# Kernel optimization log

Hardware: AMD Instinct MI355X
Metric: run time of the kernel (lower is better)

The kernel has to match this reference:

```python
import jax, jax.numpy as jnp
import numpy as np

DIM = 4096
N_HEADS = 32
N_KV_HEADS = 8
HEAD_DIM = 128
N_REP = N_HEADS // N_KV_HEADS  # 4
Q_DIM = N_HEADS * HEAD_DIM     # 4096
K_DIM = N_KV_HEADS * HEAD_DIM  # 1024
B, T = 2, 2048
ROPE_THETA = 10000.0


def setup_inputs() -> dict:
    key = jax.random.key(0)
    k1, k2, k3, k4 = jax.random.split(key, 4)
    x = jax.random.normal(k1, (B, T, DIM), dtype=jnp.float32)
    wqkv = jax.random.normal(k2, (Q_DIM + 2 * K_DIM, DIM), dtype=jnp.float32) * 0.02
    wo = jax.random.normal(k3, (DIM, DIM), dtype=jnp.float32) * 0.02
    # RoPE tables: [max_T, head_dim//2]
    inv_freq = 1.0 / (ROPE_THETA ** (jnp.arange(0, HEAD_DIM, 2, dtype=jnp.float32) / HEAD_DIM))
    angles = jnp.arange(T, dtype=jnp.float32)[:, None] * inv_freq[None, :]  # [T, D/2]
    cos = jnp.cos(angles)
    sin = jnp.sin(angles)
    freqs_cis = jax.random.normal(k4, (T, HEAD_DIM // 2), dtype=jnp.float32)  # unused by forward
    return {"x": x, "freqs_cis": freqs_cis, "wqkv": wqkv, "wo": wo, "cos": cos, "sin": sin}


def _apply_rope(q, k, cos, sin):
    # q: [B,T,Hq,D], k: [B,T,Hkv,D]; interleaved even/odd pairs
    Tlen = q.shape[1]
    c = cos[:Tlen][None, :, None, :]  # [1,T,1,D/2]
    s = sin[:Tlen][None, :, None, :]

    def rot(t):
        tr, ti = t[..., 0::2], t[..., 1::2]
        or_ = tr * c - ti * s
        oi = tr * s + ti * c
        return jnp.stack([or_, oi], axis=-1).reshape(t.shape)

    return rot(q), rot(k)


def reference(x, freqs_cis, wqkv, wo, cos, sin):
    Bx, Tx, _ = x.shape
    qkv = jnp.einsum('btd,ed->bte', x, wqkv)  # fused QKV GEMM
    q = qkv[..., :Q_DIM].reshape(Bx, Tx, N_HEADS, HEAD_DIM)
    k = qkv[..., Q_DIM:Q_DIM + K_DIM].reshape(Bx, Tx, N_KV_HEADS, HEAD_DIM)
    v = qkv[..., Q_DIM + K_DIM:].reshape(Bx, Tx, N_KV_HEADS, HEAD_DIM)
    q, k = _apply_rope(q, k, cos, sin)
    # GQA repeat_interleave over head dim
    k = jnp.repeat(k, N_REP, axis=2)  # [B,T,Hq,D]
    v = jnp.repeat(v, N_REP, axis=2)
    scale = 1.0 / jnp.sqrt(jnp.asarray(HEAD_DIM, dtype=q.dtype))
    scores = jnp.einsum('bqhd,bkhd->bhqk', q, k) * scale  # [B,H,T,T]
    causal = jnp.tril(jnp.ones((Tx, Tx), dtype=bool))
    scores = jnp.where(causal[None, None], scores, jnp.finfo(scores.dtype).min)
    probs = jax.nn.softmax(scores, axis=-1)
    y = jnp.einsum('bhqk,bkhd->bqhd', probs, v).reshape(Bx, Tx, Q_DIM)
    return jnp.einsum('btd,ed->bte', y, wo)
```

## Files before the change

### kernel.cpp

```cpp
#include <hip/hip_runtime.h>

#define T_SEQ 2048
#define NB    2
#define NH    32
#define NKV   8
#define HD    128
#define DIM   4096
#define EDIM  6144
#define M_TOK 4096

typedef __bf16          bf8  __attribute__((ext_vector_type(8)));
typedef unsigned short  us8  __attribute__((ext_vector_type(8)));
typedef float           f4   __attribute__((ext_vector_type(4)));
typedef float           f16v __attribute__((ext_vector_type(16)));
typedef int             i4   __attribute__((ext_vector_type(4)));

__device__ inline unsigned short f2bf(float f) {
  unsigned int u = __builtin_bit_cast(unsigned int, f);
  u += 0x7FFF + ((u >> 16) & 1);
  return (unsigned short)(u >> 16);
}
__device__ inline float bf2f(unsigned short h) {
  unsigned int u = ((unsigned int)h) << 16;
  return __builtin_bit_cast(float, u);
}
__device__ inline void gl_lds16(const void* g, void* l) {
  __builtin_amdgcn_global_load_lds(
      (const __attribute__((address_space(1))) unsigned int*)g,
      (__attribute__((address_space(3))) unsigned int*)l, 16, 0, 0);
}
__device__ inline f4 mfma16(bf8 a, bf8 b, f4 c) {
  return __builtin_amdgcn_mfma_f32_16x16x32_bf16(a, b, c, 0, 0, 0);
}
__device__ inline f16v mfma32(bf8 a, bf8 b, f16v c) {
  return __builtin_amdgcn_mfma_f32_32x32x16_bf16(a, b, c, 0, 0, 0);
}
__device__ inline unsigned cvtpk(float lo, float hi) {
  unsigned r;
  asm("v_cvt_pk_bf16_f32 %0, %1, %2" : "=v"(r) : "v"(lo), "v"(hi));
  return r;
}

__global__ void k_f2bf3(const float* __restrict__ x, const float* __restrict__ wq,
                        const float* __restrict__ wo,
                        unsigned short* __restrict__ xb, unsigned short* __restrict__ wqb,
                        unsigned short* __restrict__ wob) {
  const long n0 = (long)M_TOK * DIM / 4;
  const long n1 = (long)EDIM * DIM / 4;
  const long n2 = (long)DIM * DIM / 4;
  const long total = n0 + n1 + n2;
  const long stride = (long)gridDim.x * blockDim.x;
  for (long i = (long)blockIdx.x * blockDim.x + threadIdx.x; i < total; i += stride) {
    const float* in; unsigned short* out; long j = i;
    if (j < n0)              { in = x;  out = xb; }
    else if ((j -= n0) < n1) { in = wq; out = wqb; }
    else       { j -= n1;      in = wo; out = wob; }
    f4 v = *(const f4*)(in + j * 4);
    unsigned long long pack =
        (unsigned long long)f2bf(v[0]) |
        ((unsigned long long)f2bf(v[1]) << 16) |
        ((unsigned long long)f2bf(v[2]) << 32) |
        ((unsigned long long)f2bf(v[3]) << 48);
    *(unsigned long long*)(out + j * 4) = pack;
  }
}

__global__ __launch_bounds__(512, 2)
void k_gemm384(const unsigned short* __restrict__ A, const unsigned short* __restrict__ Bm,
               unsigned short* __restrict__ oQ, unsigned short* __restrict__ oK,
               unsigned short* __restrict__ oV) {
  __shared__ unsigned short As[2][8192];
  __shared__ unsigned short Bs[2][3][8192];
  const int nbx = EDIM / 384;
  const int nwg = nbx * (M_TOK / 128);
  const int n0 = blockIdx.x;
  const int q8 = nwg >> 3, r8 = nwg & 7;
  const int xcd = n0 & 7, ix = n0 >> 3;
  const int swzb = (xcd < r8 ? xcd * (q8 + 1) : r8 * (q8 + 1) + (xcd - r8) * q8) + ix;
  const int bn = swzb % nbx, bm = swzb / nbx;
  const int t = threadIdx.x;
  const int lane = t & 63, w = t >> 6;
  const int wr = w >> 2, wc = w & 3;
  const int l15 = lane & 15, lhi = lane >> 4;
  const int KT = DIM >> 6;

  f4 acc[4][6] = {};

  const int tt0 = t * 8;
  auto stA = [&](int buf, int tile) {
    if (tile >= KT) return;
    const unsigned short* gp = A + (size_t)(bm * 128) * DIM + tile * 64;
#pragma unroll
    for (int j = 0; j < 2; ++j) {
      int e = j * 4096 + tt0;
      int rl = e >> 6, cs = (e & 63) ^ ((rl & 7) << 3);
      gl_lds16(gp + (size_t)rl * DIM + cs, &As[buf][e]);
    }
  };
  auto stB = [&](int buf, int bh, int tile) {
    if (tile >= KT) return;
    const unsigned short* gp = Bm + (size_t)(bn * 384 + bh * 128) * DIM + tile * 64;
#pragma unroll
    for (int j = 0; j < 2; ++j) {
      int e = j * 4096 + tt0;
      int rl = e >> 6, cs = (e & 63) ^ ((rl & 7) << 3);
      gl_lds16(gp + (size_t)rl * DIM + cs, &Bs[buf][bh][e]);
    }
  };
  auto rdA = [&](int buf, int mi, int kk) -> bf8 {
    int row = wr * 64 + mi * 16 + l15;
    int col = (lhi * 8 + kk * 32) ^ ((row & 7) << 3);
    return __builtin_bit_cast(bf8, *(const us8*)&As[buf][row * 64 + col]);
  };
  auto rdB = [&](int buf, int bh, int ni, int kk) -> bf8 {
    int row = wc * 32 + ni * 16 + l15;
    int col = (lhi * 8 + kk * 32) ^ ((row & 7) << 3);
    return __builtin_bit_cast(bf8, *(const us8*)&Bs[buf][bh][row * 64 + col]);
  };
  auto bar = [&]() {
    asm volatile("" ::: "memory");
    __builtin_amdgcn_s_barrier();
    asm volatile("" ::: "memory");
  };
  auto lgkm0 = [&]() {
    asm volatile("s_waitcnt lgkmcnt(0)" ::: "memory");
    __builtin_amdgcn_sched_barrier(0);
  };

  stA(0, 0); stB(0, 0, 0); stB(0, 1, 0); stB(0, 2, 0);
  asm volatile("s_waitcnt vmcnt(4)" ::: "memory");
  bar();

  for (int tp = 0; tp < KT; tp += 2) {
#pragma unroll
    for (int sub = 0; sub < 2; ++sub) {
      const int tc = tp + sub, b = sub;
      const bool last = (tc == KT - 1);
      bf8 af[4][2], bfr[2][2];
#pragma unroll
      for (int mi = 0; mi < 4; ++mi)
#pragma unroll
        for (int kk = 0; kk < 2; ++kk) af[mi][kk] = rdA(b, mi, kk);
#pragma unroll
      for (int ni = 0; ni < 2; ++ni)
#pragma unroll
        for (int kk = 0; kk < 2; ++kk) bfr[ni][kk] = rdB(b, 0, ni, kk);
      stA(b ^ 1, tc + 1); stB(b ^ 1, 0, tc + 1);
      asm volatile("s_waitcnt lgkmcnt(8)" ::: "memory");
      bar(); lgkm0();
      __builtin_amdgcn_s_setprio(1);
#pragma unroll
      for (int mi = 0; mi < 4; ++mi)
#pragma unroll
        for (int ni = 0; ni < 2; ++ni)
#pragma unroll
          for (int kk = 0; kk < 2; ++kk)
            acc[mi][ni] = mfma16(af[mi][kk], bfr[ni][kk], acc[mi][ni]);
      __builtin_amdgcn_s_setprio(0);
      if (last) { asm volatile("s_waitcnt vmcnt(2)" ::: "memory"); }
      else      { asm volatile("s_waitcnt vmcnt(6)" ::: "memory"); }
      bar();
#pragma unroll
      for (int ni = 0; ni < 2; ++ni)
#pragma unroll
        for (int kk = 0; kk < 2; ++kk) bfr[ni][kk] = rdB(b, 1, ni, kk);
      stB(b ^ 1, 1, tc + 1);
      bar(); lgkm0();
      __builtin_amdgcn_s_setprio(1);
#pragma unroll
      for (int mi = 0; mi < 4; ++mi)
#pragma unroll
        for (int ni = 0; ni < 2; ++ni)
#pragma unroll
          for (int kk = 0; kk < 2; ++kk)
            acc[mi][2 + ni] = mfma16(af[mi][kk], bfr[ni][kk], acc[mi][2 + ni]);
      __builtin_amdgcn_s_setprio(0);
      if (last) { asm volatile("s_waitcnt vmcnt(0)" ::: "memory"); }
      else      { asm volatile("s_waitcnt vmcnt(6)" ::: "memory"); }
      bar();
#pragma unroll
      for (int ni = 0; ni < 2; ++ni)
#pragma unroll
        for (int kk = 0; kk < 2; ++kk) bfr[ni][kk] = rdB(b, 2, ni, kk);
      stB(b ^ 1, 2, tc + 1);
      bar(); lgkm0();
      __builtin_amdgcn_s_setprio(1);
#pragma unroll
      for (int mi = 0; mi < 4; ++mi)
#pragma unroll
        for (int ni = 0; ni < 2; ++ni)
#pragma unroll
          for (int kk = 0; kk < 2; ++kk)
            acc[mi][4 + ni] = mfma16(af[mi][kk], bfr[ni][kk], acc[mi][4 + ni]);
      __builtin_amdgcn_s_setprio(0);
      if (!last) { asm volatile("s_waitcnt vmcnt(4)" ::: "memory"); }
      bar();
    }
  }

#pragma unroll
  for (int bh = 0; bh < 3; ++bh)
#pragma unroll
    for (int ni = 0; ni < 2; ++ni) {
      const int colb = bn * 384 + bh * 128 + wc * 32 + ni * 16;
      unsigned short* op; int ldo, c0;
      if (colb < 4096)      { op = oQ; ldo = 4096; c0 = colb; }
      else if (colb < 5120) { op = oK; ldo = 1024; c0 = colb - 4096; }
      else                  { op = oV; ldo = 1024; c0 = colb - 5120; }
#pragma unroll
      for (int mi = 0; mi < 4; ++mi)
#pragma unroll
        for (int rr = 0; rr < 4; ++rr) {
          int row = bm * 128 + wr * 64 + mi * 16 + lhi * 4 + rr;
          op[(size_t)row * ldo + c0 + l15] = f2bf(acc[mi][bh * 2 + ni][rr]);
        }
    }
}

#define MFMA_Q(a0, b0, AF, BF)                                        \
  __builtin_amdgcn_s_setprio(1);                                      \
  _Pragma("unroll") for (int mi = 0; mi < 4; ++mi)                    \
  _Pragma("unroll") for (int ni = 0; ni < 2; ++ni)                    \
  _Pragma("unroll") for (int kk = 0; kk < 2; ++kk)                    \
      acc[(a0) + mi][(b0) + ni] =                                     \
          mfma16(AF[mi][kk], BF[ni][kk], acc[(a0) + mi][(b0) + ni]);  \
  __builtin_amdgcn_s_setprio(0);

#define RD_A(buf, mh)                                                 \
  _Pragma("unroll") for (int mi = 0; mi < 4; ++mi)                    \
  _Pragma("unroll") for (int kk = 0; kk < 2; ++kk)                    \
      af[mi][kk] = rdA(buf, mh, mi, kk);

#define RD_B(buf, nh, BF)                                             \
  _Pragma("unroll") for (int ni = 0; ni < 2; ++ni)                    \
  _Pragma("unroll") for (int kk = 0; kk < 2; ++kk)                    \
      BF[ni][kk] = rdB(buf, nh, ni, kk);

__global__ __launch_bounds__(512, 2)
void k_gemm256f(const unsigned short* __restrict__ A, const unsigned short* __restrict__ Bm,
                int M, int N, int K, float* __restrict__ oF) {
  __shared__ unsigned short As[2][16384];
  __shared__ unsigned short Bs[2][16384];
  const int nbx = N >> 8;
  const int nwg = nbx * (M >> 8);
  const int n0 = blockIdx.x;
  const int q8 = nwg >> 3, r8 = nwg & 7;
  const int xcd = n0 & 7, ix = n0 >> 3;
  const int swzb = (xcd < r8 ? xcd * (q8 + 1) : r8 * (q8 + 1) + (xcd - r8) * q8) + ix;
  const int bn = swzb % nbx, bm = swzb / nbx;
  const int t = threadIdx.x;
  const int lane = t & 63, w = t >> 6;
  const int wr = w >> 2, wc = w & 3;
  const int l15 = lane & 15, lhi = lane >> 4;
  const int KT = K >> 6;
  const int NI = KT >> 1;

  f4 acc[8][4] = {};

  const int tt0 = t * 8;
  auto stA = [&](int buf, int half, int tile) {
    if (tile >= KT) return;
    const unsigned short* gp = A + (size_t)(bm * 256 + half * 128) * K + tile * 64;
#pragma unroll
    for (int j = 0; j < 2; ++j) {
      int e = j * 4096 + tt0;
      int rl = e >> 6;
      int cs = (e & 63) ^ ((rl & 7) << 3);
      gl_lds16(gp + (size_t)rl * K + cs, &As[buf][half * 8192 + e]);
    }
  };
  auto stB = [&](int buf, int half, int tile) {
    if (tile >= KT) return;
    const unsigned short* gp = Bm + (size_t)(bn * 256 + half * 128) * K + tile * 64;
#pragma unroll
    for (int j = 0; j < 2; ++j) {
      int e = j * 4096 + tt0;
      int rl = e >> 6;
      int cs = (e & 63) ^ ((rl & 7) << 3);
      gl_lds16(gp + (size_t)rl * K + cs, &Bs[buf][half * 8192 + e]);
    }
  };
  auto rdA = [&](int buf, int mh, int mi, int kk) -> bf8 {
    int row = mh * 128 + wr * 64 + mi * 16 + l15;
    int col = (lhi * 8 + kk * 32) ^ ((row & 7) << 3);
    return __builtin_bit_cast(bf8, *(const us8*)&As[buf][row * 64 + col]);
  };
  auto rdB = [&](int buf, int nh, int ni, int kk) -> bf8 {
    int row = nh * 128 + wc * 32 + ni * 16 + l15;
    int col = (lhi * 8 + kk * 32) ^ ((row & 7) << 3);
    return __builtin_bit_cast(bf8, *(const us8*)&Bs[buf][row * 64 + col]);
  };
  auto bar = [&]() {
    asm volatile("" ::: "memory");
    __builtin_amdgcn_s_barrier();
    asm volatile("" ::: "memory");
  };
  auto lgkm0 = [&]() {
    asm volatile("s_waitcnt lgkmcnt(0)" ::: "memory");
    __builtin_amdgcn_sched_barrier(0);
  };

  stA(0, 0, 0); stB(0, 1, 0); stA(0, 1, 0); stB(0, 0, 0);
  stA(1, 0, 1); stB(1, 1, 1); stA(1, 1, 1);
  asm volatile("s_waitcnt vmcnt(6)" ::: "memory");
  bar();

  for (int i = 0; i < NI; ++i) {
    const int t2 = 2 * i + 2, t3 = 2 * i + 3;
    bf8 af[4][2], bf0[2][2], bf1[2][2];
    RD_A(0, 0); RD_B(0, 0, bf0);
    stB(1, 0, 2 * i + 1);
    asm volatile("s_waitcnt lgkmcnt(8)" ::: "memory");
    bar(); lgkm0();
    MFMA_Q(0, 0, af, bf0);
    bar();
    RD_B(0, 1, bf1);
    stA(0, 0, t2);
    bar(); lgkm0();
    MFMA_Q(0, 2, af, bf1);
    bar();
    RD_A(0, 1);
    stB(0, 1, t2);
    bar(); lgkm0();
    MFMA_Q(4, 2, af, bf1);
    bar();
    RD_B(0, 0, bf0);
    stA(0, 1, t2);
    bar(); lgkm0();
    MFMA_Q(4, 0, af, bf0);
    if (i + 1 < NI) { asm volatile("s_waitcnt vmcnt(6)" ::: "memory"); }
    else            { asm volatile("s_waitcnt vmcnt(0)" ::: "memory"); }
    bar();
    RD_A(1, 0); RD_B(1, 0, bf0);
    stB(0, 0, t2);
    asm volatile("s_waitcnt lgkmcnt(8)" ::: "memory");
    bar(); lgkm0();
    MFMA_Q(0, 0, af, bf0);
    bar();
    RD_B(1, 1, bf1);
    stA(1, 0, t3);
    bar(); lgkm0();
    MFMA_Q(0, 2, af, bf1);
    bar();
    RD_A(1, 1);
    stB(1, 1, t3);
    bar(); lgkm0();
    MFMA_Q(4, 2, af, bf1);
    bar();
    RD_B(1, 0, bf0);
    stA(1, 1, t3);
    bar(); lgkm0();
    MFMA_Q(4, 0, af, bf0);
    if (i + 1 < NI) { asm volatile("s_waitcnt vmcnt(6)" ::: "memory"); }
    bar();
  }

  const int rb0 = bm * 256 + wr * 64 + lhi * 4;
  const int cb0 = bn * 256 + wc * 32 + l15;
#pragma unroll
  for (int ai = 0; ai < 8; ++ai)
#pragma unroll
    for (int bj = 0; bj < 4; ++bj)
#pragma unroll
      for (int rr = 0; rr < 4; ++rr) {
        int row = rb0 + (ai >> 2) * 128 + (ai & 3) * 16 + rr;
        int col = cb0 + (bj >> 1) * 128 + (bj & 1) * 16;
        oF[(size_t)row * N + col] = acc[ai][bj][rr];
      }
}

__global__ void k_rope(unsigned short* __restrict__ Qb, unsigned short* __restrict__ Kb,
                       const float* __restrict__ cosp, const float* __restrict__ sinp) {
  const float QSCALE = (float)(0.08838834764831845 * 1.4426950408889634);
  int idx = blockIdx.x * blockDim.x + threadIdx.x;
  const int nq = M_TOK * NH * 16;
  const int nk = M_TOK * NKV * 16;
  unsigned short* p; int tpos, pg; float sc;
  if (idx < nq) {
    int m = idx >> 9;
    int r = idx & 511;
    int h = r >> 4; pg = r & 15;
    tpos = m & (T_SEQ - 1);
    p = Qb + (size_t)m * 4096 + h * 128 + pg * 8;
    sc = QSCALE;
  } else {
    idx -= nq;
    if (idx >= nk) return;
    int m = idx >> 7;
    int r = idx & 127;
    int h = r >> 4; pg = r & 15;
    tpos = m & (T_SEQ - 1);
    p = Kb + (size_t)m * 1024 + h * 128 + pg * 8;
    sc = 1.0f;
  }
  us8 v = *(const us8*)p;
  f4 c = *(const f4*)(cosp + tpos * 64 + pg * 4);
  f4 s = *(const f4*)(sinp + tpos * 64 + pg * 4);
  us8 o;
#pragma unroll
  for (int j = 0; j < 4; ++j) {
    float cs = c[j] * sc, ss = s[j] * sc;
    float tr = bf2f(v[2 * j]), ti = bf2f(v[2 * j + 1]);
    o[2 * j]     = f2bf(tr * cs - ti * ss);
    o[2 * j + 1] = f2bf(tr * ss + ti * cs);
  }
  *(us8*)p = o;
}

__global__ __launch_bounds__(512, 2)
void k_attn(const unsigned short* __restrict__ Qb, const unsigned short* __restrict__ Kb,
            const unsigned short* __restrict__ Vb, unsigned short* __restrict__ Yb) {
  __shared__ unsigned short Ks[64 * 128];
  __shared__ unsigned short Vt[128 * 64];
  const int idx = blockIdx.x;
  const int qblk = 7 - (idx >> 6);
  const int h = (idx & 63) >> 1;
  const int b = idx & 1;
  const int kvh = h >> 2;
  const int t = threadIdx.x;
  const int lane = t & 63, w = t >> 6;
  const int l31 = lane & 31, hh = lane >> 5;
  const int qb0 = qblk * 256;
  const int NT = (qblk + 1) * 4;
  const int wqmin = qb0 + w * 32;
  const int q_g = wqmin + l31;
  const float BNEG = -1.0e30f;

  bf8 qf[8];
  {
    const unsigned short* qp = Qb + (size_t)(b * T_SEQ + q_g) * 4096 + h * 128 + hh * 8;
#pragma unroll
    for (int st = 0; st < 8; ++st) qf[st] = __builtin_bit_cast(bf8, *(const us8*)(qp + st * 16));
  }
  const int swz = (l31 & 7) << 3;
  float m_run = BNEG, l_run = 0.f;
  f16v yacc[4] = {};

  const int eo0 = t * 8;
  for (int kt = 0; kt < NT; ++kt) {
    const int kbase = kt * 64;
    const unsigned short* vp = Vb + (size_t)(b * T_SEQ + kbase + lane) * 1024 + kvh * 128 + w * 8;
    us8 vv0 = *(const us8*)vp;
    us8 vv1 = *(const us8*)(vp + 64);
    __syncthreads();
#pragma unroll
    for (int i = 0; i < 2; ++i) {
      int eo = i * 4096 + eo0;
      int row = eo >> 7;
      int colL = (eo & 127) ^ ((row & 7) << 3);
      gl_lds16(Kb + (size_t)(b * T_SEQ + kbase + row) * 1024 + kvh * 128 + colL, &Ks[eo]);
    }
#pragma unroll
    for (int j = 0; j < 8; ++j) {
      int d0 = w * 8 + j;
      Vt[(d0 * 64 + lane) ^ ((d0 & 7) << 3)] = vv0[j];
      int d1 = d0 + 64;
      Vt[(d1 * 64 + lane) ^ ((d1 & 7) << 3)] = vv1[j];
    }
    __syncthreads();
    if (kbase > wqmin + 31) continue;

    f16v s0 = {}, s1 = {};
#pragma unroll
    for (int st = 0; st < 8; ++st) {
      int coff = st * 16 + hh * 8;
      bf8 a0 = __builtin_bit_cast(bf8, *(const us8*)&Ks[(l31 * 128 + coff) ^ swz]);
      bf8 a1 = __builtin_bit_cast(bf8, *(const us8*)&Ks[((l31 + 32) * 128 + coff) ^ swz]);
      s0 = mfma32(a0, qf[st], s0);
      s1 = mfma32(a1, qf[st], s1);
    }
    if (kbase + 63 > wqmin) {
#pragma unroll
      for (int r = 0; r < 16; ++r) {
        int kv = kbase + (r & 3) + 8 * (r >> 2) + 4 * hh;
        if (kv > q_g)      s0[r] = BNEG;
        if (kv + 32 > q_g) s1[r] = BNEG;
      }
    }
    float tmax = BNEG;
#pragma unroll
    for (int r = 0; r < 16; ++r) {
      tmax = fmaxf(tmax, s0[r]);
      tmax = fmaxf(tmax, s1[r]);
    }
    tmax = fmaxf(tmax, __shfl_xor(tmax, 32));
    float m_new = fmaxf(m_run, tmax);
    float fac = exp2f(m_run - m_new);
    m_run = m_new;
    float psum = 0.f;
#pragma unroll
    for (int r = 0; r < 16; ++r) {
      s0[r] = exp2f(s0[r] - m_new); psum += s0[r];
      s1[r] = exp2f(s1[r] - m_new); psum += s1[r];
    }
    psum += __shfl_xor(psum, 32);
    l_run = l_run * fac + psum;
    if (!__all(fac == 1.0f)) {
      float facr[16];
#pragma unroll
      for (int r = 0; r < 16; ++r)
        facr[r] = __shfl(fac, (r & 3) + 8 * (r >> 2) + 4 * hh);
#pragma unroll
      for (int dc = 0; dc < 4; ++dc)
#pragma unroll
        for (int r = 0; r < 16; ++r) yacc[dc][r] *= facr[r];
    }
#pragma unroll
    for (int st = 0; st < 4; ++st) {
      f16v sv = (st & 2) ? s1 : s0;
      const int rb = (st & 1) * 8;
      unsigned pkA = cvtpk(sv[rb + 0], sv[rb + 1]);
      unsigned pkB = cvtpk(sv[rb + 2], sv[rb + 3]);
      unsigned pkC = cvtpk(sv[rb + 4], sv[rb + 5]);
      unsigned pkD = cvtpk(sv[rb + 6], sv[rb + 7]);
      unsigned xA = __shfl_xor(pkA, 32);
      unsigned xB = __shfl_xor(pkB, 32);
      unsigned xC = __shfl_xor(pkC, 32);
      unsigned xD = __shfl_xor(pkD, 32);
      unsigned w0 = hh ? xC : pkA;
      unsigned w1 = hh ? xD : pkB;
      unsigned w2 = hh ? pkC : xA;
      unsigned w3 = hh ? pkD : xB;
      i4 wi = { (int)w0, (int)w1, (int)w2, (int)w3 };
      bf8 pf = __builtin_bit_cast(bf8, wi);
#pragma unroll
      for (int dc = 0; dc < 4; ++dc) {
        int d = dc * 32 + l31;
        bf8 vf = __builtin_bit_cast(bf8, *(const us8*)&Vt[(d * 64 + st * 16 + hh * 8) ^ swz]);
        yacc[dc] = mfma32(pf, vf, yacc[dc]);
      }
    }
  }
  float inv_l = 1.0f / l_run;
  float il[16];
#pragma unroll
  for (int r = 0; r < 16; ++r)
    il[r] = __shfl(inv_l, (r & 3) + 8 * (r >> 2) + 4 * hh);
#pragma unroll
  for (int dc = 0; dc < 4; ++dc)
#pragma unroll
    for (int r = 0; r < 16; ++r) {
      int qrow = qb0 + w * 32 + (r & 3) + 8 * (r >> 2) + 4 * hh;
      Yb[(size_t)(b * T_SEQ + qrow) * 4096 + h * 128 + dc * 32 + l31] =
          f2bf(yacc[dc][r] * il[r]);
    }
}

extern "C" void kernel_launch(void* const* d_in, const int* in_sizes, int n_in,
                              void* d_out, int out_size, void* d_ws, size_t ws_size,
                              hipStream_t stream) {
  const float* x    = (const float*)d_in[0];
  const float* wqkv = (const float*)d_in[2];
  const float* wo   = (const float*)d_in[3];
  const float* cosp = (const float*)d_in[4];
  const float* sinp = (const float*)d_in[5];
  float* out = (float*)d_out;

  char* ws = (char*)d_ws;
  size_t o = 0;
  auto alloc = [&](size_t bytes) { void* p = ws + o; o += (bytes + 255) & ~(size_t)255; return p; };
  unsigned short* x_b    = (unsigned short*)alloc((size_t)M_TOK * DIM * 2);
  unsigned short* wqkv_b = (unsigned short*)alloc((size_t)EDIM * DIM * 2);
  unsigned short* wo_b   = (unsigned short*)alloc((size_t)DIM * DIM * 2);
  unsigned short* Qb     = (unsigned short*)alloc((size_t)M_TOK * 4096 * 2);
  unsigned short* Kb     = (unsigned short*)alloc((size_t)M_TOK * 1024 * 2);
  unsigned short* Vb     = (unsigned short*)alloc((size_t)M_TOK * 1024 * 2);
  unsigned short* Yb     = (unsigned short*)alloc((size_t)M_TOK * 4096 * 2);
  if (o > ws_size) return;

  k_f2bf3<<<2048, 256, 0, stream>>>(x, wqkv, wo, x_b, wqkv_b, wo_b);

  k_gemm384<<<dim3(512), 512, 0, stream>>>(x_b, wqkv_b, Qb, Kb, Vb);

  k_rope<<<(M_TOK * NH * 16 + M_TOK * NKV * 16 + 255) / 256, 256, 0, stream>>>(
      Qb, Kb, cosp, sinp);

  k_attn<<<dim3(512, 1, 1), 512, 0, stream>>>(Qb, Kb, Vb, Yb);

  k_gemm256f<<<dim3(256), 512, 0, stream>>>(Yb, wo_b, M_TOK, DIM, DIM, out);
}
```

Measured before the change: 528.3 us.

## Fuse RoPE into attention, remap GEMM tile swizzle, drop redundant B reread

Removes the standalone RoPE kernel. RoPE and the Q scale are now applied while loading Q fragments, and while staging K tiles into LDS inside the attention kernel. K staging moves from direct global-to-LDS loads to register loads plus a rotate and an LDS store. The K rotation is recomputed for every query block and head that shares the KV head. Both GEMMs replace the generic XCD swizzle with a fixed 2D block mapping per XCD, and the output GEMM drops a redundant B-fragment reread and its LDS wait.

```diff
diff --git a/kernel.cpp b/kernel.cpp
--- a/kernel.cpp
+++ b/kernel.cpp
@@ -71,13 +71,10 @@
                unsigned short* __restrict__ oV) {
   __shared__ unsigned short As[2][8192];
   __shared__ unsigned short Bs[2][3][8192];
-  const int nbx = EDIM / 384;
-  const int nwg = nbx * (M_TOK / 128);
   const int n0 = blockIdx.x;
-  const int q8 = nwg >> 3, r8 = nwg & 7;
-  const int xcd = n0 & 7, ix = n0 >> 3;
-  const int swzb = (xcd < r8 ? xcd * (q8 + 1) : r8 * (q8 + 1) + (xcd - r8) * q8) + ix;
-  const int bn = swzb % nbx, bm = swzb / nbx;
+  const int x = n0 & 7, ix = n0 >> 3;
+  const int bm = ((x >> 1) << 3) + (ix >> 3);
+  const int bn = ((x & 1) << 3) + (ix & 7);
   const int t = threadIdx.x;
   const int lane = t & 63, w = t >> 6;
   const int wr = w >> 2, wc = w & 3;
@@ -238,16 +235,14 @@
 
 __global__ __launch_bounds__(512, 2)
 void k_gemm256f(const unsigned short* __restrict__ A, const unsigned short* __restrict__ Bm,
-                int M, int N, int K, float* __restrict__ oF) {
+                float* __restrict__ oF) {
   __shared__ unsigned short As[2][16384];
   __shared__ unsigned short Bs[2][16384];
-  const int nbx = N >> 8;
-  const int nwg = nbx * (M >> 8);
   const int n0 = blockIdx.x;
-  const int q8 = nwg >> 3, r8 = nwg & 7;
-  const int xcd = n0 & 7, ix = n0 >> 3;
-  const int swzb = (xcd < r8 ? xcd * (q8 + 1) : r8 * (q8 + 1) + (xcd - r8) * q8) + ix;
-  const int bn = swzb % nbx, bm = swzb / nbx;
+  const int x = n0 & 7, ix = n0 >> 3;
+  const int bm = ((x >> 1) << 2) + (ix >> 3);
+  const int bn = ((x & 1) << 3) + (ix & 7);
+  const int N = DIM, K = DIM;
   const int t = threadIdx.x;
   const int lane = t & 63, w = t >> 6;
   const int wr = w >> 2, wc = w & 3;
@@ -324,9 +319,8 @@
     bar(); lgkm0();
     MFMA_Q(4, 2, af, bf1);
     bar();
-    RD_B(0, 0, bf0);
     stA(0, 1, t2);
-    bar(); lgkm0();
+    bar();
     MFMA_Q(4, 0, af, bf0);
     if (i + 1 < NI) { asm volatile("s_waitcnt vmcnt(6)" ::: "memory"); }
     else            { asm volatile("s_waitcnt vmcnt(0)" ::: "memory"); }
@@ -347,9 +341,8 @@
     bar(); lgkm0();
     MFMA_Q(4, 2, af, bf1);
     bar();
-    RD_B(1, 0, bf0);
     stA(1, 1, t3);
-    bar(); lgkm0();
+    bar();
     MFMA_Q(4, 0, af, bf0);
     if (i + 1 < NI) { asm volatile("s_waitcnt vmcnt(6)" ::: "memory"); }
     bar();
@@ -369,47 +362,10 @@
       }
 }
 
-__global__ void k_rope(unsigned short* __restrict__ Qb, unsigned short* __restrict__ Kb,
-                       const float* __restrict__ cosp, const float* __restrict__ sinp) {
-  const float QSCALE = (float)(0.08838834764831845 * 1.4426950408889634);
-  int idx = blockIdx.x * blockDim.x + threadIdx.x;
-  const int nq = M_TOK * NH * 16;
-  const int nk = M_TOK * NKV * 16;
-  unsigned short* p; int tpos, pg; float sc;
-  if (idx < nq) {
-    int m = idx >> 9;
-    int r = idx & 511;
-    int h = r >> 4; pg = r & 15;
-    tpos = m & (T_SEQ - 1);
-    p = Qb + (size_t)m * 4096 + h * 128 + pg * 8;
-    sc = QSCALE;
-  } else {
-    idx -= nq;
-    if (idx >= nk) return;
-    int m = idx >> 7;
-    int r = idx & 127;
-    int h = r >> 4; pg = r & 15;
-    tpos = m & (T_SEQ - 1);
-    p = Kb + (size_t)m * 1024 + h * 128 + pg * 8;
-    sc = 1.0f;
-  }
-  us8 v = *(const us8*)p;
-  f4 c = *(const f4*)(cosp + tpos * 64 + pg * 4);
-  f4 s = *(const f4*)(sinp + tpos * 64 + pg * 4);
-  us8 o;
-#pragma unroll
-  for (int j = 0; j < 4; ++j) {
-    float cs = c[j] * sc, ss = s[j] * sc;
-    float tr = bf2f(v[2 * j]), ti = bf2f(v[2 * j + 1]);
-    o[2 * j]     = f2bf(tr * cs - ti * ss);
-    o[2 * j + 1] = f2bf(tr * ss + ti * cs);
-  }
-  *(us8*)p = o;
-}
-
 __global__ __launch_bounds__(512, 2)
 void k_attn(const unsigned short* __restrict__ Qb, const unsigned short* __restrict__ Kb,
-            const unsigned short* __restrict__ Vb, unsigned short* __restrict__ Yb) {
+            const unsigned short* __restrict__ Vb, unsigned short* __restrict__ Yb,
+            const float* __restrict__ cosp, const float* __restrict__ sinp) {
   __shared__ unsigned short Ks[64 * 128];
   __shared__ unsigned short Vt[128 * 64];
   const int idx = blockIdx.x;
@@ -425,30 +381,58 @@
   const int wqmin = qb0 + w * 32;
   const int q_g = wqmin + l31;
   const float BNEG = -1.0e30f;
+  const float QSCALE = (float)(0.08838834764831845 * 1.4426950408889634);
 
   bf8 qf[8];
   {
     const unsigned short* qp = Qb + (size_t)(b * T_SEQ + q_g) * 4096 + h * 128 + hh * 8;
 #pragma unroll
-    for (int st = 0; st < 8; ++st) qf[st] = __builtin_bit_cast(bf8, *(const us8*)(qp + st * 16));
+    for (int st = 0; st < 8; ++st) {
+      us8 v = *(const us8*)(qp + st * 16);
+      f4 c = *(const f4*)(cosp + q_g * 64 + st * 8 + hh * 4);
+      f4 s = *(const f4*)(sinp + q_g * 64 + st * 8 + hh * 4);
+      us8 o;
+#pragma unroll
+      for (int j = 0; j < 4; ++j) {
+        float tr = bf2f(v[2 * j]), ti = bf2f(v[2 * j + 1]);
+        o[2 * j]     = f2bf((tr * c[j] - ti * s[j]) * QSCALE);
+        o[2 * j + 1] = f2bf((tr * s[j] + ti * c[j]) * QSCALE);
+      }
+      qf[st] = __builtin_bit_cast(bf8, o);
+    }
   }
   const int swz = (l31 & 7) << 3;
   float m_run = BNEG, l_run = 0.f;
   f16v yacc[4] = {};
 
-  const int eo0 = t * 8;
+  const int krow = t >> 4;
+  const int kcol = (t & 15) * 8;
   for (int kt = 0; kt < NT; ++kt) {
     const int kbase = kt * 64;
     const unsigned short* vp = Vb + (size_t)(b * T_SEQ + kbase + lane) * 1024 + kvh * 128 + w * 8;
     us8 vv0 = *(const us8*)vp;
     us8 vv1 = *(const us8*)(vp + 64);
+    const unsigned short* kp = Kb + (size_t)(b * T_SEQ + kbase + krow) * 1024 + kvh * 128 + kcol;
+    us8 kk0 = *(const us8*)kp;
+    us8 kk1 = *(const us8*)(kp + (size_t)32 * 1024);
+    f4 kc0 = *(const f4*)(cosp + (kbase + krow) * 64 + (kcol >> 1));
+    f4 ks0 = *(const f4*)(sinp + (kbase + krow) * 64 + (kcol >> 1));
+    f4 kc1 = *(const f4*)(cosp + (kbase + krow + 32) * 64 + (kcol >> 1));
+    f4 ks1 = *(const f4*)(sinp + (kbase + krow + 32) * 64 + (kcol >> 1));
     __syncthreads();
-#pragma unroll
-    for (int i = 0; i < 2; ++i) {
-      int eo = i * 4096 + eo0;
-      int row = eo >> 7;
-      int colL = (eo & 127) ^ ((row & 7) << 3);
-      gl_lds16(Kb + (size_t)(b * T_SEQ + kbase + row) * 1024 + kvh * 128 + colL, &Ks[eo]);
+    {
+      us8 o0, o1;
+#pragma unroll
+      for (int j = 0; j < 4; ++j) {
+        float tr0 = bf2f(kk0[2 * j]), ti0 = bf2f(kk0[2 * j + 1]);
+        o0[2 * j]     = f2bf(tr0 * kc0[j] - ti0 * ks0[j]);
+        o0[2 * j + 1] = f2bf(tr0 * ks0[j] + ti0 * kc0[j]);
+        float tr1 = bf2f(kk1[2 * j]), ti1 = bf2f(kk1[2 * j + 1]);
+        o1[2 * j]     = f2bf(tr1 * kc1[j] - ti1 * ks1[j]);
+        o1[2 * j + 1] = f2bf(tr1 * ks1[j] + ti1 * kc1[j]);
+      }
+      *(us8*)&Ks[krow * 128 + (kcol ^ ((krow & 7) << 3))] = o0;
+      *(us8*)&Ks[(krow + 32) * 128 + (kcol ^ ((krow & 7) << 3))] = o1;
     }
 #pragma unroll
     for (int j = 0; j < 8; ++j) {
@@ -572,10 +556,7 @@
 
   k_gemm384<<<dim3(512), 512, 0, stream>>>(x_b, wqkv_b, Qb, Kb, Vb);
 
-  k_rope<<<(M_TOK * NH * 16 + M_TOK * NKV * 16 + 255) / 256, 256, 0, stream>>>(
-      Qb, Kb, cosp, sinp);
-
-  k_attn<<<dim3(512, 1, 1), 512, 0, stream>>>(Qb, Kb, Vb, Yb);
-
-  k_gemm256f<<<dim3(256), 512, 0, stream>>>(Yb, wo_b, M_TOK, DIM, DIM, out);
-}
+  k_attn<<<dim3(512, 1, 1), 512, 0, stream>>>(Qb, Kb, Vb, Yb, cosp, sinp);
+
+  k_gemm256f<<<dim3(256), 512, 0, stream>>>(Yb, wo_b, out);
+}
```

Measured after the change: 525.9 us. No clear change (-0.5%).
